# Kernel tuning notes

Measured on AMD Instinct MI355X. Metric: run time of the kernel, lower is better.

The kernel has to match this reference:

```python
import jax, jax.numpy as jnp
import numpy as np

NUM_HEADS = 16
ROPE_THETA = 10000.0


def setup_inputs() -> dict:
    key = jax.random.key(0)
    k1, k2, k3 = jax.random.split(key, 3)
    B, T, C = 2, 2048, 1024
    x = jax.random.normal(k1, (B, T, C), dtype=jnp.float32)
    w_qkv = jax.random.normal(k2, (3 * C, C), dtype=jnp.float32) * 0.02
    w_out = jax.random.normal(k3, (C, C), dtype=jnp.float32) * 0.02
    return {"x": x, "w_qkv": w_qkv, "w_out": w_out}


def _apply_rope(x, cos, sin):
    # x: (B, H, T, D); interleaved complex pairs: (x[...,2i], x[...,2i+1])
    B, H, T, D = x.shape
    xp = x.reshape(B, H, T, D // 2, 2)
    xr, xi = xp[..., 0], xp[..., 1]
    # cos/sin: (T, D//2) broadcast over (B, H)
    out_r = xr * cos - xi * sin
    out_i = xr * sin + xi * cos
    return jnp.stack([out_r, out_i], axis=-1).reshape(B, H, T, D)


def reference(x, w_qkv, w_out):
    B, T, C = x.shape
    H = NUM_HEADS
    D = C // H
    scale = 1.0 / np.sqrt(D).astype(np.float32)

    qkv = x @ w_qkv.T                      # (B, T, 3C)
    q, k, v = jnp.split(qkv, 3, axis=-1)

    def to_heads(t):
        return t.reshape(B, T, H, D).transpose(0, 2, 1, 3)  # (B, H, T, D)

    q, k, v = to_heads(q), to_heads(k), to_heads(v)

    # RoPE frequencies: freqs[t, j] = t / theta^(2j/D)
    inv_freq = 1.0 / (ROPE_THETA ** (jnp.arange(0, D, 2, dtype=jnp.float32) / D))
    freqs = jnp.arange(T, dtype=jnp.float32)[:, None] * inv_freq[None, :]  # (T, D//2)
    cos, sin = jnp.cos(freqs), jnp.sin(freqs)

    q = _apply_rope(q, cos, sin)
    k = _apply_rope(k, cos, sin)

    att = jnp.einsum('bhqd,bhkd->bhqk', q, k) * scale   # (B, H, T, T)
    causal = jnp.tril(jnp.ones((T, T), dtype=bool))
    att = jnp.where(causal[None, None], att, -jnp.inf)
    att = jax.nn.softmax(att, axis=-1)
    # dropout p=0.0 (eval) -> identity

    out = jnp.einsum('bhqk,bhkd->bhqd', att, v)          # (B, H, T, D)
    out = out.transpose(0, 2, 1, 3).reshape(B, T, C)
    return out @ w_out.T
```

## Files before the change

kernel.cpp:

```cpp
#include <hip/hip_runtime.h>
#include <hip/hip_bf16.h>
#include <math.h>

#define DEV __device__ __forceinline__

typedef float  floatx4 __attribute__((ext_vector_type(4)));
typedef short  bf16x8  __attribute__((ext_vector_type(8)));
typedef short  bf16x4  __attribute__((ext_vector_type(4)));

typedef __attribute__((address_space(1))) void gvoid;
typedef __attribute__((address_space(3))) void lvoid;

static constexpr int Bc = 2, Tc = 2048, Cc = 1024, Hc = 16, Dc = 64;

DEV void gload16(const void* g, void* l) {
    __builtin_amdgcn_global_load_lds((gvoid*)g, (lvoid*)l, 16, 0, 0);
}

__global__ void prep_kernel(const float* __restrict__ xf,
                            const float* __restrict__ wqkvf,
                            const float* __restrict__ woutf,
                            __hip_bfloat16* __restrict__ xb,
                            __hip_bfloat16* __restrict__ wqkvb,
                            __hip_bfloat16* __restrict__ woutb,
                            float* __restrict__ cosT, float* __restrict__ sinT) {
    int gb = blockIdx.x;
    if (gb < 8192) {
        const float* src; __hip_bfloat16* dst; int i;
        if (gb < 4096)      { src = xf;    dst = xb;    i = gb * 256 + threadIdx.x; }
        else if (gb < 7168) { src = wqkvf; dst = wqkvb; i = (gb - 4096) * 256 + threadIdx.x; }
        else                { src = woutf; dst = woutb; i = (gb - 7168) * 256 + threadIdx.x; }
        float4 f = ((const float4*)src)[i];
        union { ushort4 u; __hip_bfloat16 h[4]; } pk;
        pk.h[0] = __float2bfloat16(f.x);
        pk.h[1] = __float2bfloat16(f.y);
        pk.h[2] = __float2bfloat16(f.z);
        pk.h[3] = __float2bfloat16(f.w);
        ((ushort4*)dst)[i] = pk.u;
    } else {
        int i = (gb - 8192) * 256 + threadIdx.x;
        int t = i >> 5, j = i & 31;
        float invf = powf(10000.0f, -(float)j / 32.0f);
        float f = (float)t * invf;
        cosT[i] = cosf(f);
        sinT[i] = sinf(f);
    }
}

__global__ __launch_bounds__(256, 2) void gemm_qkv(
    const __hip_bfloat16* __restrict__ A,
    const __hip_bfloat16* __restrict__ Bm,
    __hip_bfloat16* __restrict__ qb,
    __hip_bfloat16* __restrict__ kb,
    __hip_bfloat16* __restrict__ vb,
    const float* __restrict__ cosT,
    const float* __restrict__ sinT,
    int K)
{
    __shared__ __align__(16) __hip_bfloat16 SM[2 * 128 * 64];
    __hip_bfloat16* const As = SM;
    __hip_bfloat16* const Bs = SM + 128 * 64;

    const int tid  = threadIdx.x;
    const int lane = tid & 63, wave = tid >> 6;
    const int quad = lane >> 4, cidx = lane & 15;
    const int wm = wave & 1, wn = wave >> 1;
    const int bm = blockIdx.x * 128, bn = blockIdx.y * 128;

    floatx4 acc[4][4] = {};

    for (int k0 = 0; k0 < K; k0 += 64) {
#pragma unroll
        for (int it = 0; it < 4; ++it) {
            int idx = tid + it * 256;
            int r = idx >> 3, cs = idx & 7;
            int cg = cs ^ (r & 7);
            gload16(A  + (size_t)(bm + r) * K + k0 + cg * 8, As + idx * 8);
            gload16(Bm + (size_t)(bn + r) * K + k0 + cg * 8, Bs + idx * 8);
        }
        __syncthreads();
#pragma unroll
        for (int ks = 0; ks < 2; ++ks) {
            bf16x8 af[4], bf[4];
#pragma unroll
            for (int mt = 0; mt < 4; ++mt) {
                int r = wm * 64 + mt * 16 + cidx;
                af[mt] = *(const bf16x8*)(As + (r * 8 + ((ks * 4 + quad) ^ (r & 7))) * 8);
            }
#pragma unroll
            for (int nt = 0; nt < 4; ++nt) {
                int r = wn * 64 + nt * 16 + cidx;
                bf[nt] = *(const bf16x8*)(Bs + (r * 8 + ((ks * 4 + quad) ^ (r & 7))) * 8);
            }
#pragma unroll
            for (int mt = 0; mt < 4; ++mt)
#pragma unroll
                for (int nt = 0; nt < 4; ++nt)
                    acc[mt][nt] = __builtin_amdgcn_mfma_f32_16x16x32_bf16(
                        af[mt], bf[nt], acc[mt][nt], 0, 0, 0);
        }
        __syncthreads();
    }

    if (bn >= 2048) {
#pragma unroll
        for (int nt = 0; nt < 4; ++nt) {
            int n_l = wn * 64 + nt * 16 + cidx;
#pragma unroll
            for (int mt = 0; mt < 4; ++mt)
#pragma unroll
                for (int reg = 0; reg < 4; ++reg) {
                    int m_l = wm * 64 + mt * 16 + quad * 4 + reg;
                    SM[n_l * 128 + (((m_l >> 3) ^ (n_l & 15)) * 8) + (m_l & 7)] =
                        __float2bfloat16(acc[mt][nt][reg]);
                }
        }
        __syncthreads();
        {
            int b = bm >> 11, t0 = bm & 2047;
            int c = tid & 15;
#pragma unroll
            for (int it = 0; it < 8; ++it) {
                int row = it * 16 + (tid >> 4);
                int cc = (bn - 2048) + row;
                int h = cc >> 6, d = cc & 63;
                *(uint4*)(vb + ((size_t)(b * Hc + h) * Dc + d) * Tc + t0 + c * 8) =
                    *(const uint4*)(SM + row * 128 + ((c ^ (row & 15)) * 8));
            }
        }
    } else {
        const float SL2E = 0.125f * 1.44269504088896f;
#pragma unroll
        for (int nt = 0; nt < 4; ++nt) {
            int n   = bn + wn * 64 + nt * 16 + cidx;
            int sec = n >> 10;
            int cc  = n & 1023;
            int h = cc >> 6, d = cc & 63, j = d >> 1;
            __hip_bfloat16* dst = (sec == 0) ? qb : kb;
#pragma unroll
            for (int mt = 0; mt < 4; ++mt) {
#pragma unroll
                for (int reg = 0; reg < 4; ++reg) {
                    int m = bm + wm * 64 + mt * 16 + quad * 4 + reg;
                    int b = m >> 11, t = m & 2047;
                    float v = acc[mt][nt][reg];
                    float p = __shfl_xor(v, 1);
                    float cz = cosT[t * 32 + j];
                    float sz = sinT[t * 32 + j];
                    float o = (d & 1) ? (p * sz + v * cz) : (v * cz - p * sz);
                    if (sec == 0) o *= SL2E;
                    dst[((size_t)(b * Hc + h) * Tc + t) * Dc + d] = __float2bfloat16(o);
                }
            }
        }
    }
}

__global__ __launch_bounds__(256, 2) void gemm_out(
    const __hip_bfloat16* __restrict__ A,
    const __hip_bfloat16* __restrict__ Bm,
    float* __restrict__ Cout)
{
    __shared__ __align__(16) __hip_bfloat16 As[64 * 64];
    __shared__ __align__(16) __hip_bfloat16 Bs[128 * 64];

    const int tid  = threadIdx.x;
    const int lane = tid & 63, wave = tid >> 6;
    const int quad = lane >> 4, cidx = lane & 15;
    const int bm = blockIdx.x * 64, bn = blockIdx.y * 128;
    const int K = 1024;

    floatx4 acc[4][2] = {};

    for (int k0 = 0; k0 < K; k0 += 64) {
        int h = k0 >> 6;
#pragma unroll
        for (int it = 0; it < 2; ++it) {
            int idx = tid + it * 256;
            int r = idx >> 3, cs = idx & 7;
            int cg = cs ^ (r & 7);
            int m = bm + r;
            const __hip_bfloat16* src =
                A + ((size_t)((m >> 11) * 16 + h) * 2048 + (m & 2047)) * 64 + cg * 8;
            gload16(src, As + idx * 8);
        }
#pragma unroll
        for (int it = 0; it < 4; ++it) {
            int idx = tid + it * 256;
            int r = idx >> 3, cs = idx & 7;
            int cg = cs ^ (r & 7);
            gload16(Bm + (size_t)(bn + r) * K + k0 + cg * 8, Bs + idx * 8);
        }
        __syncthreads();
#pragma unroll
        for (int ks = 0; ks < 2; ++ks) {
            bf16x8 af[4], bf[2];
#pragma unroll
            for (int mt = 0; mt < 4; ++mt) {
                int r = mt * 16 + cidx;
                af[mt] = *(const bf16x8*)(As + (r * 8 + ((ks * 4 + quad) ^ (r & 7))) * 8);
            }
#pragma unroll
            for (int nt = 0; nt < 2; ++nt) {
                int r = wave * 32 + nt * 16 + cidx;
                bf[nt] = *(const bf16x8*)(Bs + (r * 8 + ((ks * 4 + quad) ^ (r & 7))) * 8);
            }
#pragma unroll
            for (int mt = 0; mt < 4; ++mt)
#pragma unroll
                for (int nt = 0; nt < 2; ++nt)
                    acc[mt][nt] = __builtin_amdgcn_mfma_f32_16x16x32_bf16(
                        af[mt], bf[nt], acc[mt][nt], 0, 0, 0);
        }
        __syncthreads();
    }

#pragma unroll
    for (int mt = 0; mt < 4; ++mt)
#pragma unroll
        for (int nt = 0; nt < 2; ++nt) {
            int n = bn + wave * 32 + nt * 16 + cidx;
#pragma unroll
            for (int reg = 0; reg < 4; ++reg) {
                int m = bm + mt * 16 + quad * 4 + reg;
                Cout[(size_t)m * 1024 + n] = acc[mt][nt][reg];
            }
        }
}

__global__ __launch_bounds__(256, 2) void attn_kernel(
    const __hip_bfloat16* __restrict__ qb,
    const __hip_bfloat16* __restrict__ kb,
    const __hip_bfloat16* __restrict__ vb,
    __hip_bfloat16* __restrict__ ob)
{
    __shared__ __align__(16) __hip_bfloat16 Ks[128 * 64];
    __shared__ __align__(16) __hip_bfloat16 Vt[64 * 128];
    __shared__ __align__(16) __hip_bfloat16 Ps[128 * 64];
    __shared__ float Ls[4][64];

    const int tid  = threadIdx.x;
    const int lane = tid & 63, wave = tid >> 6;
    const int quad = lane >> 4, cidx = lane & 15;
    const int id = blockIdx.x;
    const int xcd = id & 7, s = id >> 3;
    const int bh = xcd * 4 + (s >> 4);
    const int bx = s & 15;
    const size_t plane = (size_t)bh * Tc * Dc;
    const __hip_bfloat16* Vp = vb + plane;

    for (int half = 0; half < 2; ++half) {
        const int qt = half ? bx : 31 - bx;
        const int qbase = qt * 64;
        const int ktmax = (qbase + 63) >> 7;

#pragma unroll
        for (int it = 0; it < 2; ++it) {
            int idx = tid + it * 256;
            int r = idx >> 3, cs = idx & 7;
            int cg = cs ^ (r & 7);
            gload16(qb + plane + (size_t)(qbase + r) * 64 + cg * 8, Vt + idx * 8);
        }
#pragma unroll
        for (int it = 0; it < 4; ++it) {
            int idx = tid + it * 256;
            int r = idx >> 3, cs = idx & 7;
            int cg = cs ^ (r & 7);
            gload16(kb + plane + (size_t)r * 64 + cg * 8, Ks + idx * 8);
        }
        __syncthreads();
        bf16x8 qf[4][2];
#pragma unroll
        for (int mt = 0; mt < 4; ++mt)
#pragma unroll
            for (int ks = 0; ks < 2; ++ks) {
                int r = mt * 16 + cidx;
                qf[mt][ks] = *(const bf16x8*)(Vt + (r * 8 + ((ks * 4 + quad) ^ (r & 7))) * 8);
            }
        __syncthreads();

        floatx4 oaccT[4][4] = {};
        float lsum[4] = {0.f, 0.f, 0.f, 0.f};

        for (int kt = 0; kt <= ktmax; ++kt) {
#pragma unroll
            for (int it = 0; it < 4; ++it) {
                int idx = tid + it * 256;
                int r = idx >> 4, cs = idx & 15;
                int c = cs ^ (r & 15);
                gload16(Vp + (size_t)r * Tc + kt * 128 + c * 8, Vt + idx * 8);
            }

            floatx4 sacc[4][2] = {};
#pragma unroll
            for (int ks = 0; ks < 2; ++ks) {
                bf16x8 kf[2];
#pragma unroll
                for (int nt2 = 0; nt2 < 2; ++nt2) {
                    int r = wave * 32 + nt2 * 16 + cidx;
                    kf[nt2] = *(const bf16x8*)(Ks + (r * 8 + ((ks * 4 + quad) ^ (r & 7))) * 8);
                }
#pragma unroll
                for (int mt = 0; mt < 4; ++mt)
#pragma unroll
                    for (int nt2 = 0; nt2 < 2; ++nt2)
                        sacc[mt][nt2] = __builtin_amdgcn_mfma_f32_16x16x32_bf16(
                            kf[nt2], qf[mt][ks], sacc[mt][nt2], 0, 0, 0);
            }

            const bool domask = (kt == ktmax);
            bf16x4 pf[4][2];
#pragma unroll
            for (int mt = 0; mt < 4; ++mt) {
                int q = qbase + mt * 16 + cidx;
#pragma unroll
                for (int nt2 = 0; nt2 < 2; ++nt2) {
#pragma unroll
                    for (int reg = 0; reg < 4; ++reg) {
                        int key = kt * 128 + wave * 32 + nt2 * 16 + quad * 4 + reg;
                        float p = __builtin_amdgcn_exp2f(sacc[mt][nt2][reg]);
                        if (domask && key > q) p = 0.0f;
                        lsum[mt] += p;
                        __hip_bfloat16 hb = __float2bfloat16(p);
                        pf[mt][nt2][reg] = *(const short*)&hb;
                    }
                }
            }

            __syncthreads();

            if (kt < ktmax) {
#pragma unroll
                for (int it = 0; it < 4; ++it) {
                    int idx = tid + it * 256;
                    int r = idx >> 3, cs = idx & 7;
                    int cg = cs ^ (r & 7);
                    gload16(kb + plane + (size_t)((kt + 1) * 128 + r) * 64 + cg * 8,
                            Ks + idx * 8);
                }
            }

#pragma unroll
            for (int dt = 0; dt < 4; ++dt) {
                int d = dt * 16 + cidx;
#pragma unroll
                for (int ks2 = 0; ks2 < 2; ++ks2) {
                    int chunk = wave * 4 + ks2 * 2 + (quad >> 1);
                    bf16x4 vtf = *(const bf16x4*)(
                        Vt + (d * 16 + (chunk ^ (d & 15))) * 8 + (quad & 1) * 4);
#pragma unroll
                    for (int mt = 0; mt < 4; ++mt)
                        oaccT[mt][dt] = __builtin_amdgcn_mfma_f32_16x16x16bf16_1k(
                            vtf, pf[mt][ks2], oaccT[mt][dt], 0, 0, 0);
                }
            }
            __syncthreads();
        }

#pragma unroll
        for (int off = 16; off < 64; off <<= 1)
#pragma unroll
            for (int mt = 0; mt < 4; ++mt)
                lsum[mt] += __shfl_xor(lsum[mt], off);
        if (quad == 0)
#pragma unroll
            for (int mt = 0; mt < 4; ++mt)
                Ls[wave][mt * 16 + cidx] = lsum[mt];

        if (wave != 0) {
            float* dstw = (wave == 1) ? (float*)Ks : (wave == 2) ? (float*)Vt : (float*)Ps;
#pragma unroll
            for (int mt = 0; mt < 4; ++mt)
#pragma unroll
                for (int dt = 0; dt < 4; ++dt)
                    ((floatx4*)dstw)[(mt * 4 + dt) * 64 + lane] = oaccT[mt][dt];
        }
        __syncthreads();
        if (wave == 0) {
#pragma unroll
            for (int mt = 0; mt < 4; ++mt)
#pragma unroll
                for (int dt = 0; dt < 4; ++dt) {
                    int i = (mt * 4 + dt) * 64 + lane;
                    oaccT[mt][dt] += ((const floatx4*)Ks)[i];
                    oaccT[mt][dt] += ((const floatx4*)Vt)[i];
                    oaccT[mt][dt] += ((const floatx4*)Ps)[i];
                }
#pragma unroll
            for (int mt = 0; mt < 4; ++mt) {
                int q = mt * 16 + cidx;
                float lt = Ls[0][q] + Ls[1][q] + Ls[2][q] + Ls[3][q];
                float inv = 1.0f / lt;
#pragma unroll
                for (int dt = 0; dt < 4; ++dt) {
                    bf16x4 o4;
#pragma unroll
                    for (int reg = 0; reg < 4; ++reg) {
                        __hip_bfloat16 hb = __float2bfloat16(oaccT[mt][dt][reg] * inv);
                        o4[reg] = *(const short*)&hb;
                    }
                    int g = dt * 4 + quad;
                    *(bf16x4*)(Ks + q * 64 + (g ^ (q & 12)) * 4) = o4;
                }
            }
        }
        __syncthreads();
#pragma unroll
        for (int i = 0; i < 2; ++i) {
            int c = tid * 2 + i;
            int row = c >> 3, cp = c & 7;
            *(uint4*)(ob + plane + (size_t)(qbase + row) * 64 + cp * 8) =
                *(const uint4*)(Ks + row * 64 + ((cp * 2) ^ (row & 12)) * 4);
        }
        __syncthreads();
    }
}

extern "C" void kernel_launch(void* const* d_in, const int* in_sizes, int n_in,
                              void* d_out, int out_size, void* d_ws, size_t ws_size,
                              hipStream_t stream) {
    const float* xf = nullptr; const float* wqkvf = nullptr; const float* woutf = nullptr;
    for (int i = 0; i < n_in; ++i) {
        if      (in_sizes[i] == 2 * 2048 * 1024) xf    = (const float*)d_in[i];
        else if (in_sizes[i] == 3 * 1024 * 1024) wqkvf = (const float*)d_in[i];
        else if (in_sizes[i] == 1024 * 1024)     woutf = (const float*)d_in[i];
    }
    float* out = (float*)d_out;

    char* ws = (char*)d_ws;
    const size_t MB = 1024 * 1024;
    __hip_bfloat16* qb    = (__hip_bfloat16*)(ws);
    __hip_bfloat16* kb    = (__hip_bfloat16*)(ws + 8  * MB);
    __hip_bfloat16* vb    = (__hip_bfloat16*)(ws + 16 * MB);
    __hip_bfloat16* ab    = (__hip_bfloat16*)(ws + 24 * MB);
    float* cosT           = (float*)(ws + 32 * MB);
    float* sinT           = (float*)(ws + 32 * MB + 256 * 1024);
    __hip_bfloat16* xb    = (__hip_bfloat16*)(ws + 33 * MB);
    __hip_bfloat16* wqkvb = (__hip_bfloat16*)(ws + 41 * MB);
    __hip_bfloat16* woutb = (__hip_bfloat16*)(ws + 47 * MB);

    prep_kernel<<<dim3(8448), dim3(256), 0, stream>>>(
        xf, wqkvf, woutf, xb, wqkvb, woutb, cosT, sinT);

    gemm_qkv<<<dim3(32, 24), dim3(256), 0, stream>>>(
        xb, wqkvb, qb, kb, vb, cosT, sinT, 1024);
    attn_kernel<<<dim3(512), dim3(256), 0, stream>>>(qb, kb, vb, ab);
    gemm_out<<<dim3(64, 8), dim3(256), 0, stream>>>(ab, woutb, out);
}
```

Measured before the change: 176.5 us.

## Load K fragments directly to registers and double-buffer V tiles in LDS

In the attention kernel, K is no longer staged through shared memory. Each wave loads its K MFMA fragments straight from global memory into registers, prefetching the next tile's fragments while it works on the current one. V tiles are double-buffered in LDS so the next tile's async load overlaps the current PV MFMAs, which leaves one barrier per iteration instead of two. Launch bounds rise to 3 blocks per CU. The trade-off is higher register pressure from the prefetched K fragments and uncoalesced per-lane global K reads, which could cause spills under the tighter register budget.

```diff
diff --git a/kernel.cpp b/kernel.cpp
--- a/kernel.cpp
+++ b/kernel.cpp
@@ -228,14 +228,13 @@
         }
 }
 
-__global__ __launch_bounds__(256, 2) void attn_kernel(
+__global__ __launch_bounds__(256, 3) void attn_kernel(
     const __hip_bfloat16* __restrict__ qb,
     const __hip_bfloat16* __restrict__ kb,
     const __hip_bfloat16* __restrict__ vb,
     __hip_bfloat16* __restrict__ ob)
 {
-    __shared__ __align__(16) __hip_bfloat16 Ks[128 * 64];
-    __shared__ __align__(16) __hip_bfloat16 Vt[64 * 128];
+    __shared__ __align__(16) __hip_bfloat16 Vt[2][64 * 128];
     __shared__ __align__(16) __hip_bfloat16 Ps[128 * 64];
     __shared__ float Ls[4][64];
 
@@ -248,6 +247,7 @@
     const int bx = s & 15;
     const size_t plane = (size_t)bh * Tc * Dc;
     const __hip_bfloat16* Vp = vb + plane;
+    const __hip_bfloat16* Kp = kb + plane;
 
     for (int half = 0; half < 2; ++half) {
         const int qt = half ? bx : 31 - bx;
@@ -259,54 +259,67 @@
             int idx = tid + it * 256;
             int r = idx >> 3, cs = idx & 7;
             int cg = cs ^ (r & 7);
-            gload16(qb + plane + (size_t)(qbase + r) * 64 + cg * 8, Vt + idx * 8);
-        }
+            gload16(qb + plane + (size_t)(qbase + r) * 64 + cg * 8, &Vt[0][idx * 8]);
+        }
+        bf16x8 kcur[2][2];
+#pragma unroll
+        for (int nt2 = 0; nt2 < 2; ++nt2)
+#pragma unroll
+            for (int ks = 0; ks < 2; ++ks)
+                kcur[nt2][ks] = *(const bf16x8*)(
+                    Kp + (size_t)(wave * 32 + nt2 * 16 + cidx) * 64 + (ks * 4 + quad) * 8);
+        __syncthreads();
+        bf16x8 qf[4][2];
+#pragma unroll
+        for (int mt = 0; mt < 4; ++mt)
+#pragma unroll
+            for (int ks = 0; ks < 2; ++ks) {
+                int r = mt * 16 + cidx;
+                qf[mt][ks] = *(const bf16x8*)(&Vt[0][(r * 8 + ((ks * 4 + quad) ^ (r & 7))) * 8]);
+            }
+        __syncthreads();
 #pragma unroll
         for (int it = 0; it < 4; ++it) {
             int idx = tid + it * 256;
-            int r = idx >> 3, cs = idx & 7;
-            int cg = cs ^ (r & 7);
-            gload16(kb + plane + (size_t)r * 64 + cg * 8, Ks + idx * 8);
-        }
-        __syncthreads();
-        bf16x8 qf[4][2];
-#pragma unroll
-        for (int mt = 0; mt < 4; ++mt)
-#pragma unroll
-            for (int ks = 0; ks < 2; ++ks) {
-                int r = mt * 16 + cidx;
-                qf[mt][ks] = *(const bf16x8*)(Vt + (r * 8 + ((ks * 4 + quad) ^ (r & 7))) * 8);
-            }
-        __syncthreads();
+            int r = idx >> 4, cs = idx & 15;
+            int c = cs ^ (r & 15);
+            gload16(Vp + (size_t)r * Tc + c * 8, &Vt[0][idx * 8]);
+        }
 
         floatx4 oaccT[4][4] = {};
         float lsum[4] = {0.f, 0.f, 0.f, 0.f};
 
         for (int kt = 0; kt <= ktmax; ++kt) {
-#pragma unroll
-            for (int it = 0; it < 4; ++it) {
-                int idx = tid + it * 256;
-                int r = idx >> 4, cs = idx & 15;
-                int c = cs ^ (r & 15);
-                gload16(Vp + (size_t)r * Tc + kt * 128 + c * 8, Vt + idx * 8);
+            __syncthreads();
+
+            bf16x8 knxt[2][2];
+            if (kt < ktmax) {
+                __hip_bfloat16* dstb = &Vt[(kt + 1) & 1][0];
+#pragma unroll
+                for (int it = 0; it < 4; ++it) {
+                    int idx = tid + it * 256;
+                    int r = idx >> 4, cs = idx & 15;
+                    int c = cs ^ (r & 15);
+                    gload16(Vp + (size_t)r * Tc + (kt + 1) * 128 + c * 8, dstb + idx * 8);
+                }
+#pragma unroll
+                for (int nt2 = 0; nt2 < 2; ++nt2)
+#pragma unroll
+                    for (int ks = 0; ks < 2; ++ks)
+                        knxt[nt2][ks] = *(const bf16x8*)(
+                            Kp + (size_t)((kt + 1) * 128 + wave * 32 + nt2 * 16 + cidx) * 64
+                               + (ks * 4 + quad) * 8);
             }
 
             floatx4 sacc[4][2] = {};
 #pragma unroll
-            for (int ks = 0; ks < 2; ++ks) {
-                bf16x8 kf[2];
-#pragma unroll
-                for (int nt2 = 0; nt2 < 2; ++nt2) {
-                    int r = wave * 32 + nt2 * 16 + cidx;
-                    kf[nt2] = *(const bf16x8*)(Ks + (r * 8 + ((ks * 4 + quad) ^ (r & 7))) * 8);
-                }
+            for (int ks = 0; ks < 2; ++ks)
 #pragma unroll
                 for (int mt = 0; mt < 4; ++mt)
 #pragma unroll
                     for (int nt2 = 0; nt2 < 2; ++nt2)
                         sacc[mt][nt2] = __builtin_amdgcn_mfma_f32_16x16x32_bf16(
-                            kf[nt2], qf[mt][ks], sacc[mt][nt2], 0, 0, 0);
-            }
+                            kcur[nt2][ks], qf[mt][ks], sacc[mt][nt2], 0, 0, 0);
 
             const bool domask = (kt == ktmax);
             bf16x4 pf[4][2];
@@ -327,19 +340,7 @@
                 }
             }
 
-            __syncthreads();
-
-            if (kt < ktmax) {
-#pragma unroll
-                for (int it = 0; it < 4; ++it) {
-                    int idx = tid + it * 256;
-                    int r = idx >> 3, cs = idx & 7;
-                    int cg = cs ^ (r & 7);
-                    gload16(kb + plane + (size_t)((kt + 1) * 128 + r) * 64 + cg * 8,
-                            Ks + idx * 8);
-                }
-            }
-
+            const __hip_bfloat16* vbuf = &Vt[kt & 1][0];
 #pragma unroll
             for (int dt = 0; dt < 4; ++dt) {
                 int d = dt * 16 + cidx;
@@ -347,15 +348,20 @@
                 for (int ks2 = 0; ks2 < 2; ++ks2) {
                     int chunk = wave * 4 + ks2 * 2 + (quad >> 1);
                     bf16x4 vtf = *(const bf16x4*)(
-                        Vt + (d * 16 + (chunk ^ (d & 15))) * 8 + (quad & 1) * 4);
+                        vbuf + (d * 16 + (chunk ^ (d & 15))) * 8 + (quad & 1) * 4);
 #pragma unroll
                     for (int mt = 0; mt < 4; ++mt)
                         oaccT[mt][dt] = __builtin_amdgcn_mfma_f32_16x16x16bf16_1k(
                             vtf, pf[mt][ks2], oaccT[mt][dt], 0, 0, 0);
                 }
             }
-            __syncthreads();
-        }
+#pragma unroll
+            for (int nt2 = 0; nt2 < 2; ++nt2)
+#pragma unroll
+                for (int ks = 0; ks < 2; ++ks)
+                    kcur[nt2][ks] = knxt[nt2][ks];
+        }
+        __syncthreads();
 
 #pragma unroll
         for (int off = 16; off < 64; off <<= 1)
@@ -368,7 +374,8 @@
                 Ls[wave][mt * 16 + cidx] = lsum[mt];
 
         if (wave != 0) {
-            float* dstw = (wave == 1) ? (float*)Ks : (wave == 2) ? (float*)Vt : (float*)Ps;
+            float* dstw = (wave == 1) ? (float*)&Vt[0][0]
+                        : (wave == 2) ? (float*)&Vt[1][0] : (float*)Ps;
 #pragma unroll
             for (int mt = 0; mt < 4; ++mt)
 #pragma unroll
@@ -382,8 +389,8 @@
 #pragma unroll
                 for (int dt = 0; dt < 4; ++dt) {
                     int i = (mt * 4 + dt) * 64 + lane;
-                    oaccT[mt][dt] += ((const floatx4*)Ks)[i];
-                    oaccT[mt][dt] += ((const floatx4*)Vt)[i];
+                    oaccT[mt][dt] += ((const floatx4*)&Vt[0][0])[i];
+                    oaccT[mt][dt] += ((const floatx4*)&Vt[1][0])[i];
                     oaccT[mt][dt] += ((const floatx4*)Ps)[i];
                 }
 #pragma unroll
@@ -400,7 +407,7 @@
                         o4[reg] = *(const short*)&hb;
                     }
                     int g = dt * 4 + quad;
-                    *(bf16x4*)(Ks + q * 64 + (g ^ (q & 12)) * 4) = o4;
+                    *(bf16x4*)(Ps + q * 64 + (g ^ (q & 12)) * 4) = o4;
                 }
             }
         }
@@ -410,7 +417,7 @@
             int c = tid * 2 + i;
             int row = c >> 3, cp = c & 7;
             *(uint4*)(ob + plane + (size_t)(qbase + row) * 64 + cp * 8) =
-                *(const uint4*)(Ks + row * 64 + ((cp * 2) ^ (row & 12)) * 4);
+                *(const uint4*)(Ps + row * 64 + ((cp * 2) ^ (row & 12)) * 4);
         }
         __syncthreads();
     }
```

New measurement: 213.7 us. 1.21x slower.
